# Kernel tuning notes

Hardware: AMD Instinct MI355X
Metric: run time of the kernel (lower is better)

## Reference

```python
import jax, jax.numpy as jnp
import numpy as np

WINDOW = (2, 6, 12)  # (Wz, Wh, Ww), N = 144
HEADS = 6
TYPE_OF_WINDOWS = 10


def _position_index(ws):
    Wz, Wh, Ww = ws
    zi = np.arange(Wz); zj = -np.arange(Wz) * Wz
    hi = np.arange(Wh); hj = -np.arange(Wh) * Wh
    w = np.arange(Ww)
    c1 = np.stack(np.meshgrid(zi, hi, w, indexing='ij')).reshape(3, -1)
    c2 = np.stack(np.meshgrid(zj, hj, w, indexing='ij')).reshape(3, -1)
    coords = (c1[:, :, None] - c2[:, None, :]).transpose(1, 2, 0).copy()
    coords[:, :, 2] += Ww - 1
    coords[:, :, 1] *= 2 * Ww - 1
    coords[:, :, 0] *= (2 * Ww - 1) * Wh * Wh
    return coords.sum(-1).reshape(-1)  # [N*N]


def setup_inputs() -> dict:
    key = jax.random.key(0)
    ks = jax.random.split(key, 7)
    B, nW, C = 96, TYPE_OF_WINDOWS, 192
    N = WINDOW[0] * WINDOW[1] * WINDOW[2]
    bias_len = (2 * WINDOW[2] - 1) * WINDOW[1] ** 2 * WINDOW[0] ** 2
    return {
        'x': jax.random.normal(ks[0], (B, nW, N, C), jnp.float32),
        'mask': jax.random.normal(ks[1], (B, N, N), jnp.float32),
        'w_qkv': jax.random.normal(ks[2], (C, 3 * C), jnp.float32) * 0.02,
        'b_qkv': jnp.zeros((3 * C,), jnp.float32),
        'w_proj': jax.random.normal(ks[3], (C, C), jnp.float32) * 0.02,
        'b_proj': jnp.zeros((C,), jnp.float32),
        'bias_table': jax.random.normal(ks[4], (bias_len, nW, HEADS), jnp.float32) * 0.02,
        'position_index': jnp.asarray(_position_index(WINDOW), jnp.int32),
    }


def reference(x, mask, w_qkv, b_qkv, w_proj, b_proj, bias_table, position_index):
    B, nW, N, C = x.shape
    H = HEADS
    Dh = C // H
    scale = Dh ** -0.5
    qkv = x @ w_qkv + b_qkv                       # [B,nW,N,3C]
    qkv = qkv.reshape(B, nW, N, 3, H, Dh)
    qkv = qkv.transpose(3, 0, 1, 4, 2, 5)         # [3,B,nW,H,N,Dh]
    q, k, v = qkv[0], qkv[1], qkv[2]
    attn = jnp.einsum('bwhnd,bwhmd->bwhnm', q * scale, k)   # [B,nW,H,N,N]
    bias = bias_table[position_index]             # [N*N,nW,H]
    bias = bias.reshape(N, N, nW, H).transpose(2, 3, 0, 1)  # [nW,H,N,N]
    attn = attn + bias[None] + mask[:, None, None, :, :]
    attn = jax.nn.softmax(attn, axis=-1)
    out = jnp.einsum('bwhnm,bwhmd->bwhnd', attn, v)         # [B,nW,H,N,Dh]
    out = out.transpose(0, 1, 3, 2, 4).reshape(B, nW, N, C)
    return out @ w_proj + b_proj
```

## Files before the change

kernel.cpp:

```cpp
#include <hip/hip_runtime.h>
#include <math.h>

#define B_   96
#define NW   10
#define NN   144
#define CC   192
#define HH   6
#define DH   32
#define SCALE 0.17677669529663687f

#define XP 200
#define PP 152
#define NBW (B_ * NW)
#define QKV_STRIDE (NN * DH)

typedef __attribute__((ext_vector_type(8))) short v8s;
typedef __attribute__((ext_vector_type(4))) unsigned short v4us;
typedef __attribute__((ext_vector_type(4))) float v4f;

__device__ __forceinline__ unsigned short f2b(float f) {
  union { float f; unsigned u; } v; v.f = f;
  unsigned r = v.u + 0x7fffu + ((v.u >> 16) & 1u);
  return (unsigned short)(r >> 16);
}
__device__ __forceinline__ float b2f(unsigned short s) {
  union { unsigned u; float f; } v; v.u = ((unsigned)s) << 16;
  return v.f;
}

#define N_WQT (576*192)
#define N_WPT (192*192)
#define N_BIAS (NW*HH*NN*NN)

__global__ __launch_bounds__(256) void prep_kernel(
    const float* __restrict__ w_qkv, const float* __restrict__ w_proj,
    const float* __restrict__ bias_table, const int* __restrict__ pos,
    unsigned short* __restrict__ wqT, unsigned short* __restrict__ wpT,
    unsigned short* __restrict__ biasNN)
{
  int i = blockIdx.x * 256 + threadIdx.x;
  if (i < N_WQT) {
    int n = i / 192, k = i % 192;
    wqT[i] = f2b(w_qkv[k * 576 + n]);
  } else if (i < N_WQT + N_WPT) {
    int j = i - N_WQT;
    int n = j / 192, k = j % 192;
    wpT[j] = f2b(w_proj[k * 192 + n]);
  } else if (i < N_WQT + N_WPT + N_BIAS) {
    int j = i - (N_WQT + N_WPT);
    int m = j % NN, n = (j / NN) % NN, h = (j / (NN * NN)) % HH, w = j / (NN * NN * HH);
    biasNN[j] = f2b(bias_table[(pos[n * NN + m] * NW + w) * HH + h]);
  }
}

__global__ __launch_bounds__(256, 3) void qkv_gemm(
    const float* __restrict__ x, const float* __restrict__ b_qkv,
    const unsigned short* __restrict__ wqT,
    unsigned short* __restrict__ qkv, int bw0)
{
  __shared__ unsigned short xs[48 * XP];
  const int tid  = threadIdx.x;
  const int wave = tid >> 6, lane = tid & 63;
  const int lr = lane & 15, lk8 = (lane >> 4) * 8, quad = lane >> 4;
  const int bwl = blockIdx.x / 3;
  const int rt3 = blockIdx.x % 3;
  const int bw  = bw0 + bwl;

  const float4* xp4 = (const float4*)(x + ((size_t)bw * NN + rt3 * 48) * CC);
  for (int i = tid; i < 48 * (CC / 4); i += 256) {
    float4 f = xp4[i];
    int r = i / (CC / 4), c = (i % (CC / 4)) * 4;
    unsigned short* d = &xs[r * XP + c];
    d[0] = f2b(f.x); d[1] = f2b(f.y); d[2] = f2b(f.z); d[3] = f2b(f.w);
  }
  __syncthreads();

  v8s a[3][6];
  #pragma unroll
  for (int ii = 0; ii < 3; ii++)
    #pragma unroll
    for (int ks = 0; ks < 6; ks++)
      a[ii][ks] = *(const v8s*)&xs[(ii * 16 + lr) * XP + ks * 32 + lk8];

  v8s bf0[6], bf1[6];
  {
    const unsigned short* w0 = wqT + (size_t)(wave * 16 + lr) * CC;
    #pragma unroll
    for (int ks = 0; ks < 6; ks++) bf0[ks] = *(const v8s*)&w0[ks * 32 + lk8];
  }

  #pragma unroll
  for (int i = 0; i < 9; i++) {
    const int c = wave + i * 4;
    if (i + 1 < 9) {
      const unsigned short* wn = wqT + (size_t)((c + 4) * 16 + lr) * CC;
      if (i & 1) {
        #pragma unroll
        for (int ks = 0; ks < 6; ks++) bf0[ks] = *(const v8s*)&wn[ks * 32 + lk8];
      } else {
        #pragma unroll
        for (int ks = 0; ks < 6; ks++) bf1[ks] = *(const v8s*)&wn[ks * 32 + lk8];
      }
    }

    const int s = c / 12;
    const int h = (c % 12) >> 1;
    const int dhalf = c & 1;
    const float bv = b_qkv[c * 16 + lr];
    v4f acc[3];
    #pragma unroll
    for (int ii = 0; ii < 3; ii++) acc[ii] = (v4f){bv, bv, bv, bv};
    if (i & 1) {
      #pragma unroll
      for (int ks = 0; ks < 6; ks++)
        #pragma unroll
        for (int ii = 0; ii < 3; ii++)
          acc[ii] = __builtin_amdgcn_mfma_f32_16x16x32_bf16(a[ii][ks], bf1[ks], acc[ii], 0, 0, 0);
    } else {
      #pragma unroll
      for (int ks = 0; ks < 6; ks++)
        #pragma unroll
        for (int ii = 0; ii < 3; ii++)
          acc[ii] = __builtin_amdgcn_mfma_f32_16x16x32_bf16(a[ii][ks], bf0[ks], acc[ii], 0, 0, 0);
    }

    if (s == 2) {
      unsigned short* opT = qkv + ((size_t)(bwl * HH + h) * 3 + 2) * QKV_STRIDE
                          + (size_t)(dhalf * 16 + lr) * NN;
      #pragma unroll
      for (int ii = 0; ii < 3; ii++) {
        const int n0 = rt3 * 48 + ii * 16 + quad * 4;
        v4us pk;
        #pragma unroll
        for (int r = 0; r < 4; r++) pk[r] = f2b(acc[ii][r]);
        *(v4us*)&opT[n0] = pk;
      }
    } else {
      unsigned short* op = qkv + ((size_t)(bwl * HH + h) * 3 + s) * QKV_STRIDE + dhalf * 16 + lr;
      #pragma unroll
      for (int ii = 0; ii < 3; ii++)
        #pragma unroll
        for (int r = 0; r < 4; r++) {
          const int n = rt3 * 48 + ii * 16 + quad * 4 + r;
          op[n * DH] = f2b(acc[ii][r]);
        }
    }
  }
}

__global__ __launch_bounds__(256, 2) void attn_bwh(
    const unsigned short* __restrict__ qkv, const float* __restrict__ mask,
    const unsigned short* __restrict__ biasNN,
    unsigned short* __restrict__ ao, int bw0)
{
  __shared__ unsigned short Ps[NN * PP];

  const int tid  = threadIdx.x;
  const int wave = tid >> 6, lane = tid & 63;
  const int lr = lane & 15, lk8 = (lane >> 4) * 8, quad = lane >> 4;

  const int bwl = blockIdx.x / HH;
  const int h   = blockIdx.x % HH;
  const int bw  = bw0 + bwl;
  const int b   = bw / NW;
  const int w   = bw % NW;

  const unsigned short* qp = qkv + (size_t)(bwl * HH + h) * 3 * QKV_STRIDE;
  const unsigned short* kp = qp + QKV_STRIDE;
  const unsigned short* vT = qp + 2 * QKV_STRIDE;

  v8s bv[2][4], bvt[2];
  #pragma unroll
  for (int dh2 = 0; dh2 < 2; dh2++) {
    const unsigned short* vrow = vT + (size_t)(dh2 * 16 + lr) * NN;
    #pragma unroll
    for (int ks = 0; ks < 4; ks++) bv[dh2][ks] = *(const v8s*)&vrow[ks * 32 + lk8];
    bvt[dh2] = *(const v8s*)&vrow[128 + (lk8 & 8)];
  }

  v8s aq[9];
  #pragma unroll
  for (int nt = 0; nt < 9; nt++)
    aq[nt] = *(const v8s*)&qp[(nt * 16 + lr) * DH + lk8];

  for (int mt = wave; mt < 9; mt += 4) {
    v8s bk = *(const v8s*)&kp[(mt * 16 + lr) * DH + lk8];
    const int m = mt * 16 + lr;
    #pragma unroll
    for (int nt = 0; nt < 9; nt++) {
      v4f c = {0.f, 0.f, 0.f, 0.f};
      c = __builtin_amdgcn_mfma_f32_16x16x32_bf16(aq[nt], bk, c, 0, 0, 0);
      #pragma unroll
      for (int r = 0; r < 4; r++) {
        const int n = nt * 16 + quad * 4 + r;
        Ps[n * PP + m] = f2b(c[r] * SCALE);
      }
    }
  }
  __syncthreads();

  const unsigned short* bp = biasNN + (size_t)(w * HH + h) * NN * NN;
  const float* mp = mask + (size_t)b * NN * NN;
  for (int rr = 0; rr < 9; rr++) {
    const int row = rr * 16 + wave * 4 + quad;
    unsigned short* prow = &Ps[row * PP];
    const unsigned short* brow = bp + (size_t)row * NN;
    const float* mrow = mp + (size_t)row * NN;
    float bm[9];
    #pragma unroll
    for (int j = 0; j < 9; j++)
      bm[j] = b2f(brow[j * 16 + lr]) + mrow[j * 16 + lr];
    float e[9];
    float mx = -1e30f;
    #pragma unroll
    for (int j = 0; j < 9; j++) {
      e[j] = b2f(prow[j * 16 + lr]) + bm[j];
      mx = fmaxf(mx, e[j]);
    }
    #pragma unroll
    for (int off = 8; off; off >>= 1) mx = fmaxf(mx, __shfl_xor(mx, off, 64));
    float s = 0.f;
    #pragma unroll
    for (int j = 0; j < 9; j++) { e[j] = __expf(e[j] - mx); s += e[j]; }
    #pragma unroll
    for (int off = 8; off; off >>= 1) s += __shfl_xor(s, off, 64);
    const float inv = 1.f / s;
    #pragma unroll
    for (int j = 0; j < 9; j++) prow[j * 16 + lr] = f2b(e[j] * inv);
  }
  __syncthreads();

  const v8s vzero = {};
  for (int nt = wave; nt < 9; nt += 4) {
    v8s ap[4];
    #pragma unroll
    for (int ks = 0; ks < 4; ks++)
      ap[ks] = *(const v8s*)&Ps[(nt * 16 + lr) * PP + ks * 32 + lk8];
    v8s at = *(const v8s*)&Ps[(nt * 16 + lr) * PP + 128 + (lk8 & 8)];
    at = (quad < 2) ? at : vzero;
    #pragma unroll
    for (int dh2 = 0; dh2 < 2; dh2++) {
      v4f c = {0.f, 0.f, 0.f, 0.f};
      #pragma unroll
      for (int ks = 0; ks < 4; ks++)
        c = __builtin_amdgcn_mfma_f32_16x16x32_bf16(ap[ks], bv[dh2][ks], c, 0, 0, 0);
      c = __builtin_amdgcn_mfma_f32_16x16x32_bf16(at, bvt[dh2], c, 0, 0, 0);
      #pragma unroll
      for (int r = 0; r < 4; r++) {
        const int n = nt * 16 + quad * 4 + r;
        ao[((size_t)bw * NN + n) * CC + h * DH + dh2 * 16 + lr] = f2b(c[r]);
      }
    }
  }
}

__global__ __launch_bounds__(256) void proj_mfma(
    const unsigned short* __restrict__ ao,
    const unsigned short* __restrict__ wpT,
    const float* __restrict__ b_proj,
    float* __restrict__ out)
{
  const int tid  = threadIdx.x;
  const int wave = tid >> 6, lane = tid & 63;
  const int lr = lane & 15, lk8 = (lane >> 4) * 8, quad = lane >> 4;
  const size_t row0 = (size_t)blockIdx.x * 64;
  const int j0 = wave * 3;

  v8s bf[3][6];
  #pragma unroll
  for (int jj = 0; jj < 3; jj++)
    #pragma unroll
    for (int ks = 0; ks < 6; ks++)
      bf[jj][ks] = *(const v8s*)(wpT + (size_t)((j0 + jj) * 16 + lr) * CC + ks * 32 + lk8);

  float bvj[3];
  #pragma unroll
  for (int jj = 0; jj < 3; jj++) bvj[jj] = b_proj[(j0 + jj) * 16 + lr];

  #pragma unroll
  for (int rt = 0; rt < 4; rt++) {
    const size_t r0 = row0 + rt * 16;
    v8s a[6];
    #pragma unroll
    for (int ks = 0; ks < 6; ks++)
      a[ks] = *(const v8s*)(ao + (r0 + lr) * CC + ks * 32 + lk8);
    v4f acc[3];
    #pragma unroll
    for (int jj = 0; jj < 3; jj++) acc[jj] = (v4f){bvj[jj], bvj[jj], bvj[jj], bvj[jj]};
    #pragma unroll
    for (int ks = 0; ks < 6; ks++)
      #pragma unroll
      for (int jj = 0; jj < 3; jj++)
        acc[jj] = __builtin_amdgcn_mfma_f32_16x16x32_bf16(a[ks], bf[jj][ks], acc[jj], 0, 0, 0);
    #pragma unroll
    for (int jj = 0; jj < 3; jj++)
      #pragma unroll
      for (int r = 0; r < 4; r++)
        out[(r0 + quad * 4 + r) * CC + (j0 + jj) * 16 + lr] = acc[jj][r];
  }
}

extern "C" void kernel_launch(void* const* d_in, const int* in_sizes, int n_in,
                              void* d_out, int out_size, void* d_ws, size_t ws_size,
                              hipStream_t stream)
{
  const float* x          = (const float*)d_in[0];
  const float* mask       = (const float*)d_in[1];
  const float* w_qkv      = (const float*)d_in[2];
  const float* b_qkv      = (const float*)d_in[3];
  const float* w_proj     = (const float*)d_in[4];
  const float* b_proj     = (const float*)d_in[5];
  const float* bias_table = (const float*)d_in[6];
  const int*   pos        = (const int*)d_in[7];
  float* out = (float*)d_out;

  unsigned short* biasNN = (unsigned short*)d_ws;
  unsigned short* wqT    = biasNN + N_BIAS;
  unsigned short* wpT    = wqT + N_WQT;
  unsigned short* ao     = wpT + N_WPT;
  unsigned short* qkvws  = ao + (size_t)B_ * NW * NN * CC;

  const size_t fixed_bytes = (size_t)(qkvws - (unsigned short*)d_ws) * sizeof(unsigned short);
  const size_t per_bw      = (size_t)HH * 3 * QKV_STRIDE * sizeof(unsigned short);
  size_t avail = (ws_size > fixed_bytes) ? (ws_size - fixed_bytes) : 0;
  int maxchunk = (int)(avail / per_bw);
  if (maxchunk < 60)  maxchunk = 60;
  if (maxchunk > NBW) maxchunk = NBW;
  const int npass = (NBW + maxchunk - 1) / maxchunk;
  const int chunk = (NBW + npass - 1) / npass;

  const int prep_total = N_WQT + N_WPT + N_BIAS;
  prep_kernel<<<(prep_total + 255) / 256, 256, 0, stream>>>(
      w_qkv, w_proj, bias_table, pos, wqT, wpT, biasNN);

  for (int bw0 = 0; bw0 < NBW; bw0 += chunk) {
    const int cur = (NBW - bw0 < chunk) ? (NBW - bw0) : chunk;
    qkv_gemm<<<cur * 3, 256, 0, stream>>>(x, b_qkv, wqT, qkvws, bw0);
    attn_bwh<<<cur * HH, 256, 0, stream>>>(qkvws, mask, biasNN, ao, bw0);
  }
  proj_mfma<<<(B_ * NW * NN) / 64, 256, 0, stream>>>(ao, wpT, b_proj, out);
}
```

Baseline: 488.6 us.

## Process full 144-row window per block in QKV GEMM to reuse weight fragments

The QKV GEMM block now covers all 144 rows of a window instead of a 48-row third. Each weight fragment loaded from global memory is reused across 9 row tiles rather than 3, so total weight traffic drops threefold. A-operand fragments are streamed from LDS per k-step instead of held in registers, and the x staging writes packed 4-element vectors. In exchange the grid shrinks to one block per window, LDS per block grows to about 57 KB, and the launch bound falls to 2 blocks, which lowers parallelism and occupancy.

```diff
diff --git a/kernel.cpp b/kernel.cpp
--- a/kernel.cpp
+++ b/kernel.cpp
@@ -53,34 +53,27 @@
   }
 }
 
-__global__ __launch_bounds__(256, 3) void qkv_gemm(
+__global__ __launch_bounds__(256, 2) void qkv_gemm(
     const float* __restrict__ x, const float* __restrict__ b_qkv,
     const unsigned short* __restrict__ wqT,
     unsigned short* __restrict__ qkv, int bw0)
 {
-  __shared__ unsigned short xs[48 * XP];
+  __shared__ unsigned short xs[NN * XP];
   const int tid  = threadIdx.x;
   const int wave = tid >> 6, lane = tid & 63;
   const int lr = lane & 15, lk8 = (lane >> 4) * 8, quad = lane >> 4;
-  const int bwl = blockIdx.x / 3;
-  const int rt3 = blockIdx.x % 3;
+  const int bwl = blockIdx.x;
   const int bw  = bw0 + bwl;
 
-  const float4* xp4 = (const float4*)(x + ((size_t)bw * NN + rt3 * 48) * CC);
-  for (int i = tid; i < 48 * (CC / 4); i += 256) {
+  const float4* xp4 = (const float4*)(x + (size_t)bw * NN * CC);
+  for (int i = tid; i < NN * (CC / 4); i += 256) {
     float4 f = xp4[i];
     int r = i / (CC / 4), c = (i % (CC / 4)) * 4;
-    unsigned short* d = &xs[r * XP + c];
-    d[0] = f2b(f.x); d[1] = f2b(f.y); d[2] = f2b(f.z); d[3] = f2b(f.w);
+    v4us pk;
+    pk[0] = f2b(f.x); pk[1] = f2b(f.y); pk[2] = f2b(f.z); pk[3] = f2b(f.w);
+    *(v4us*)&xs[r * XP + c] = pk;
   }
   __syncthreads();
-
-  v8s a[3][6];
-  #pragma unroll
-  for (int ii = 0; ii < 3; ii++)
-    #pragma unroll
-    for (int ks = 0; ks < 6; ks++)
-      a[ii][ks] = *(const v8s*)&xs[(ii * 16 + lr) * XP + ks * 32 + lk8];
 
   v8s bf0[6], bf1[6];
   {
@@ -107,29 +100,33 @@
     const int h = (c % 12) >> 1;
     const int dhalf = c & 1;
     const float bv = b_qkv[c * 16 + lr];
-    v4f acc[3];
-    #pragma unroll
-    for (int ii = 0; ii < 3; ii++) acc[ii] = (v4f){bv, bv, bv, bv};
-    if (i & 1) {
-      #pragma unroll
-      for (int ks = 0; ks < 6; ks++)
-        #pragma unroll
-        for (int ii = 0; ii < 3; ii++)
-          acc[ii] = __builtin_amdgcn_mfma_f32_16x16x32_bf16(a[ii][ks], bf1[ks], acc[ii], 0, 0, 0);
-    } else {
-      #pragma unroll
-      for (int ks = 0; ks < 6; ks++)
-        #pragma unroll
-        for (int ii = 0; ii < 3; ii++)
-          acc[ii] = __builtin_amdgcn_mfma_f32_16x16x32_bf16(a[ii][ks], bf0[ks], acc[ii], 0, 0, 0);
+    v4f acc[9];
+    #pragma unroll
+    for (int ii = 0; ii < 9; ii++) acc[ii] = (v4f){bv, bv, bv, bv};
+
+    #pragma unroll
+    for (int ks = 0; ks < 6; ks++) {
+      v8s at[9];
+      #pragma unroll
+      for (int ii = 0; ii < 9; ii++)
+        at[ii] = *(const v8s*)&xs[(ii * 16 + lr) * XP + ks * 32 + lk8];
+      if (i & 1) {
+        #pragma unroll
+        for (int ii = 0; ii < 9; ii++)
+          acc[ii] = __builtin_amdgcn_mfma_f32_16x16x32_bf16(at[ii], bf1[ks], acc[ii], 0, 0, 0);
+      } else {
+        #pragma unroll
+        for (int ii = 0; ii < 9; ii++)
+          acc[ii] = __builtin_amdgcn_mfma_f32_16x16x32_bf16(at[ii], bf0[ks], acc[ii], 0, 0, 0);
+      }
     }
 
     if (s == 2) {
       unsigned short* opT = qkv + ((size_t)(bwl * HH + h) * 3 + 2) * QKV_STRIDE
                           + (size_t)(dhalf * 16 + lr) * NN;
       #pragma unroll
-      for (int ii = 0; ii < 3; ii++) {
-        const int n0 = rt3 * 48 + ii * 16 + quad * 4;
+      for (int ii = 0; ii < 9; ii++) {
+        const int n0 = ii * 16 + quad * 4;
         v4us pk;
         #pragma unroll
         for (int r = 0; r < 4; r++) pk[r] = f2b(acc[ii][r]);
@@ -138,10 +135,10 @@
     } else {
       unsigned short* op = qkv + ((size_t)(bwl * HH + h) * 3 + s) * QKV_STRIDE + dhalf * 16 + lr;
       #pragma unroll
-      for (int ii = 0; ii < 3; ii++)
+      for (int ii = 0; ii < 9; ii++)
         #pragma unroll
         for (int r = 0; r < 4; r++) {
-          const int n = rt3 * 48 + ii * 16 + quad * 4 + r;
+          const int n = ii * 16 + quad * 4 + r;
           op[n * DH] = f2b(acc[ii][r]);
         }
     }
@@ -335,7 +332,7 @@
 
   for (int bw0 = 0; bw0 < NBW; bw0 += chunk) {
     const int cur = (NBW - bw0 < chunk) ? (NBW - bw0) : chunk;
-    qkv_gemm<<<cur * 3, 256, 0, stream>>>(x, b_qkv, wqT, qkvws, bw0);
+    qkv_gemm<<<cur, 256, 0, stream>>>(x, b_qkv, wqT, qkvws, bw0);
     attn_bwh<<<cur * HH, 256, 0, stream>>>(qkvws, mask, biasNN, ao, bw0);
   }
   proj_mfma<<<(B_ * NW * NN) / 64, 256, 0, stream>>>(ao, wpT, b_proj, out);
```

Measured after the change: 441.0 us. 9.7% less time.
